# Optimization experiments

Hardware: AMD Instinct MI355X
Metric: run time of the kernel (lower is better)

## Reference

```python
import jax, jax.numpy as jnp
import numpy as np

N_NODES = 20000
DIM = 512
N_EDGES = 320000  # first N_NODES edges are self-loops so every node has a predecessor
EPS = 1e-7


def _logmap0(y):
    # Poincare ball (c=1) log map at origin: artanh(||y||) * y / ||y||
    n = jnp.linalg.norm(y, axis=-1, keepdims=True)
    nc = jnp.clip(n, EPS, 1.0 - 1e-6)
    return jnp.arctanh(nc) * y / nc


def _expmap0(v):
    # Poincare ball (c=1) exp map at origin: tanh(||v||) * v / ||v||
    n = jnp.linalg.norm(v, axis=-1, keepdims=True)
    nc = jnp.maximum(n, EPS)
    return jnp.tanh(nc) * v / nc


def setup_inputs() -> dict:
    key = jax.random.key(0)
    ks = jax.random.split(key, 9)
    x_raw = jax.random.normal(ks[0], (N_NODES, DIM), dtype=jnp.float32)
    nrm = jnp.linalg.norm(x_raw, axis=-1, keepdims=True)
    x = 0.7 * x_raw / (1.0 + nrm)  # strictly inside the unit ball

    rng = np.random.RandomState(0)
    src_rand = rng.randint(0, N_NODES, size=N_EDGES - N_NODES)
    dst_rand = rng.randint(0, N_NODES, size=N_EDGES - N_NODES)
    loop = np.arange(N_NODES)
    src = jnp.asarray(np.concatenate([loop, src_rand]), dtype=jnp.int32)
    dst = jnp.asarray(np.concatenate([loop, dst_rand]), dtype=jnp.int32)

    s = 1.0 / np.sqrt(DIM)
    Wq = jax.random.normal(ks[1], (DIM, DIM), jnp.float32) * s
    bq = jax.random.normal(ks[2], (DIM,), jnp.float32) * 0.01
    Wk = jax.random.normal(ks[3], (DIM, DIM), jnp.float32) * s
    bk = jax.random.normal(ks[4], (DIM,), jnp.float32) * 0.01
    Wv = jax.random.normal(ks[5], (DIM, DIM), jnp.float32) * s
    bv = jax.random.normal(ks[6], (DIM,), jnp.float32) * 0.01
    Wo = jax.random.normal(ks[7], (DIM, DIM), jnp.float32) * s
    bo = jax.random.normal(ks[8], (DIM,), jnp.float32) * 0.01
    return dict(x=x, src=src, dst=dst, Wq=Wq, bq=bq, Wk=Wk, bk=bk,
                Wv=Wv, bv=bv, Wo=Wo, bo=bo)


def reference(x, src, dst, Wq, bq, Wk, bk, Wv, bv, Wo, bo):
    n_nodes, d = x.shape
    scale = 1.0 / jnp.sqrt(jnp.asarray(d, x.dtype))

    t = _logmap0(x)                                  # [N, d] tangent vectors
    q = (t @ Wq.T + bq) * scale                      # torch MHA scales q
    k = t @ Wk.T + bk
    v = t @ Wv.T + bv

    # Per-destination attention over predecessor (src) neighbors.
    scores = jnp.sum(q[dst] * k[src], axis=-1)       # [E]
    m = jax.ops.segment_max(scores, dst, num_segments=n_nodes)
    e = jnp.exp(scores - m[dst])
    denom = jax.ops.segment_sum(e, dst, num_segments=n_nodes)
    alpha = e / denom[dst]                           # [E] softmax weights

    attn = jax.ops.segment_sum(alpha[:, None] * v[src], dst,
                               num_segments=n_nodes)  # [N, d]
    new_h = attn @ Wo.T + bo                          # MHA output projection
    return _expmap0(new_h)
```

## Files before the change

### kernel.cpp

```cpp
#include <hip/hip_runtime.h>
#include <math.h>
#include <stdint.h>

#define NND 20000
#define DIMK 512
#define NE  320000

typedef __attribute__((ext_vector_type(8))) short short8;
typedef __attribute__((ext_vector_type(4))) float floatx4;

__device__ inline float bf2f(unsigned short h) {
    unsigned int u = ((unsigned int)h) << 16;
    return __uint_as_float(u);
}
__device__ inline unsigned short f2bf(float f) {
    unsigned int u = __float_as_uint(f);
    unsigned int r = (u + 0x7fffu + ((u >> 16) & 1u)) >> 16;
    return (unsigned short)r;
}

__device__ __forceinline__ void gld_lds16(const unsigned short* g, unsigned short* l) {
    __builtin_amdgcn_global_load_lds(
        (const __attribute__((address_space(1))) void*)g,
        (__attribute__((address_space(3))) void*)l,
        16, 0, 0);
}

__global__ __launch_bounds__(256) void k_pre(const float* __restrict__ x,
                                             const float* __restrict__ Wq,
                                             const float* __restrict__ Wk,
                                             const float* __restrict__ Wv,
                                             const float* __restrict__ Wo,
                                             const float* __restrict__ bq,
                                             const float* __restrict__ bv,
                                             const float* __restrict__ bo,
                                             const int* __restrict__ dst,
                                             int* __restrict__ counts,
                                             unsigned short* __restrict__ t,
                                             unsigned short* __restrict__ WqTs,
                                             unsigned short* __restrict__ WkT,
                                             unsigned short* __restrict__ WvT,
                                             unsigned short* __restrict__ WoB,
                                             float* __restrict__ bh,
                                             float* __restrict__ bpr,
                                             float scf) {
    int blk = blockIdx.x, tid = threadIdx.x;
    if (blk < 5000) {
        int row = blk * 4 + (tid >> 6);
        int lane = tid & 63;
        const floatx4* xp = (const floatx4*)(x + (size_t)row * DIMK + lane * 8);
        floatx4 x0 = xp[0], x1 = xp[1];
        float ss = 0.f;
#pragma unroll
        for (int i = 0; i < 4; i++) { ss += x0[i] * x0[i]; ss += x1[i] * x1[i]; }
#pragma unroll
        for (int off = 32; off >= 1; off >>= 1) ss += __shfl_xor(ss, off, 64);
        float n  = sqrtf(ss);
        float nc = fminf(fmaxf(n, 1e-7f), 1.0f - 1e-6f);
        float fac = atanhf(nc) / nc;
        union { short8 v; unsigned short u[8]; } o;
#pragma unroll
        for (int i = 0; i < 4; i++) { o.u[i] = f2bf(fac * x0[i]); o.u[4 + i] = f2bf(fac * x1[i]); }
        *(short8*)(t + (size_t)row * DIMK + lane * 8) = o.v;
    } else if (blk < 5256) {
        int i = (blk - 5000) * 256 + tid;
        floatx4 f = *(const floatx4*)(Wo + (size_t)i * 4);
        union { unsigned long long d; unsigned short u[4]; } o;
#pragma unroll
        for (int q = 0; q < 4; q++) o.u[q] = f2bf(f[q]);
        *(unsigned long long*)(WoB + (size_t)i * 4) = o.d;
    } else if (blk < 5448) {
        int g = blk - 5256;
        int m = g >> 6, tile = g & 63;
        int tr = tile >> 3, tc = tile & 7;
        const float* srcm = (m == 0) ? Wq : (m == 1) ? Wk : Wv;
        unsigned short* dstp = (m == 0) ? WqTs : (m == 1) ? WkT : WvT;
        float sc = (m == 0) ? scf : 1.0f;
        __shared__ float tl[64][65];
#pragma unroll
        for (int i = 0; i < 16; i++) {
            int idx = i * 256 + tid; int r = idx >> 6, c = idx & 63;
            tl[c][r] = srcm[(size_t)(tr * 64 + r) * 512 + tc * 64 + c];
        }
        __syncthreads();
#pragma unroll
        for (int i = 0; i < 16; i++) {
            int idx = i * 256 + tid; int r = idx >> 6, c = idx & 63;
            dstp[(size_t)(tc * 64 + r) * 512 + tr * 64 + c] = f2bf(tl[r][c] * sc);
        }
    } else if (blk < 5450) {
        int col = (blk - 5448) * 256 + tid;
        float s = 0.f;
#pragma unroll 8
        for (int m = 0; m < 512; m++) s += bq[m] * Wk[(size_t)m * 512 + col];
        bh[col] = s * scf;
    } else if (blk < 5578) {
        int row = (blk - 5450) * 4 + (tid >> 6);
        int lane = tid & 63;
        const floatx4* wp = (const floatx4*)(Wo + (size_t)row * 512 + lane * 8);
        const floatx4* bp = (const floatx4*)(bv + lane * 8);
        floatx4 a0 = wp[0], a1 = wp[1], c0 = bp[0], c1 = bp[1];
        float s = 0.f;
#pragma unroll
        for (int i = 0; i < 4; i++) { s += a0[i] * c0[i]; s += a1[i] * c1[i]; }
#pragma unroll
        for (int off = 32; off >= 1; off >>= 1) s += __shfl_xor(s, off, 64);
        if (lane == 0) bpr[row] = s + bo[row];
    } else {
        int e = (blk - 5578) * 256 + tid;
        if (e < NE) atomicAdd(&counts[dst[e]], 1);
    }
}

__global__ __launch_bounds__(256) void k_gemm(const unsigned short* __restrict__ A,
                                              const unsigned short* __restrict__ B,
                                              const float* __restrict__ biasf,
                                              unsigned short* __restrict__ out_q,
                                              float* __restrict__ out_f,
                                              int M, int MT, int NT, int Ncols) {
    __shared__ unsigned short smem[16384];
    int b = blockIdx.x;
    int xcd = b & 7, i = b >> 3;
    int nt = i % NT, mt = (i / NT) * 8 + xcd;
    if (mt >= MT) return;
    int m0 = mt * 128, n0 = nt * 128;
    int tid = threadIdx.x, wv = tid >> 6, ln = tid & 63;
    int lr = ln & 15, qd = ln >> 4;
    int mh = wv >> 1, nh = wv & 1;

    floatx4 acc[4][4] = {};
    int srow = wv * 16 + (ln >> 2);
    int scol = (((ln & 3) ^ (ln >> 4)) & 3) * 8;
    int fsw = (qd ^ (lr >> 2)) & 3;

    {
        unsigned short* Ab = smem;
        unsigned short* Bb = smem + 8192;
#pragma unroll
        for (int p = 0; p < 2; p++) {
            int tr = p * 64 + srow;
            int ar = m0 + tr; if (ar > M - 1) ar = M - 1;
            gld_lds16(A + (size_t)ar * DIMK + scol, Ab + (p * 64 + wv * 16) * 32);
            gld_lds16(B + (size_t)(n0 + tr) * DIMK + scol, Bb + (p * 64 + wv * 16) * 32);
        }
    }

    for (int it = 0; it < 16; it++) {
        int cur = it & 1, nxt = cur ^ 1;
        __syncthreads();
        if (it + 1 < 16) {
            int kb = (it + 1) * 32;
            unsigned short* Ab = smem + nxt * 4096;
            unsigned short* Bb = smem + 8192 + nxt * 4096;
#pragma unroll
            for (int p = 0; p < 2; p++) {
                int tr = p * 64 + srow;
                int ar = m0 + tr; if (ar > M - 1) ar = M - 1;
                gld_lds16(A + (size_t)ar * DIMK + kb + scol, Ab + (p * 64 + wv * 16) * 32);
                gld_lds16(B + (size_t)(n0 + tr) * DIMK + kb + scol, Bb + (p * 64 + wv * 16) * 32);
            }
        }
        const unsigned short* Ac = smem + cur * 4096;
        const unsigned short* Bc = smem + 8192 + cur * 4096;
        short8 af[4], bfr[4];
#pragma unroll
        for (int mi = 0; mi < 4; mi++)
            af[mi] = *(const short8*)(Ac + (mh * 64 + mi * 16 + lr) * 32 + fsw * 8);
#pragma unroll
        for (int ni = 0; ni < 4; ni++)
            bfr[ni] = *(const short8*)(Bc + (nh * 64 + ni * 16 + lr) * 32 + fsw * 8);
#pragma unroll
        for (int mi = 0; mi < 4; mi++)
#pragma unroll
            for (int ni = 0; ni < 4; ni++)
                acc[mi][ni] = __builtin_amdgcn_mfma_f32_16x16x32_bf16(af[mi], bfr[ni], acc[mi][ni], 0, 0, 0);
    }

    float bb[4];
#pragma unroll
    for (int ni = 0; ni < 4; ni++) bb[ni] = biasf[n0 + nh * 64 + ni * 16 + lr];

    if (!out_f) {
        int col0 = nt * 128;
        unsigned short* cs = smem;
#pragma unroll
        for (int g = 0; g < 4; g++) {
            __syncthreads();
            if (mh == (g >> 1)) {
                int miB = (g & 1) * 2;
#pragma unroll
                for (int m2 = 0; m2 < 2; m2++) {
                    int mi = miB + m2;
                    int lrow = mi * 16 + qd * 4 - (g & 1) * 32;
#pragma unroll
                    for (int ni = 0; ni < 4; ni++) {
                        int col = nh * 64 + ni * 16 + lr;
#pragma unroll
                        for (int r = 0; r < 4; r++)
                            cs[(lrow + r) * 128 + col] = f2bf(acc[mi][ni][r] + bb[ni]);
                    }
                }
            }
            __syncthreads();
#pragma unroll
            for (int itr = 0; itr < 2; itr++) {
                int slot = itr * 256 + tid;
                int row = slot >> 4, cg = slot & 15;
                int gm = m0 + g * 32 + row;
                if (gm < M) {
                    short8 vv = *(const short8*)(cs + row * 128 + cg * 8);
                    *(short8*)(out_q + (size_t)gm * 512 + col0 + cg * 8) = vv;
                }
            }
        }
    } else {
#pragma unroll
        for (int ni = 0; ni < 4; ni++) {
            int gn = n0 + nh * 64 + ni * 16 + lr;
#pragma unroll
            for (int mi = 0; mi < 4; mi++) {
                int gm0 = m0 + mh * 64 + mi * 16 + qd * 4;
#pragma unroll
                for (int r = 0; r < 4; r++) {
                    int gm = gm0 + r;
                    if (gm < M) out_f[(size_t)gm * Ncols + gn] = acc[mi][ni][r] + bb[ni];
                }
            }
        }
    }
}

__global__ __launch_bounds__(1024) void k_scan(const int* __restrict__ counts,
                                               int* __restrict__ offsets,
                                               int* __restrict__ pos) {
    const int C = 20;
    __shared__ int wsum[16];
    __shared__ int wpre[16];
    int tid = threadIdx.x, lane = tid & 63, w = tid >> 6;
    int local[C];
    int run = 0;
#pragma unroll
    for (int i = 0; i < C; i++) {
        int idx = tid * C + i;
        int c = (idx < NND) ? counts[idx] : 0;
        local[i] = run; run += c;
    }
    int v = run;
#pragma unroll
    for (int off = 1; off < 64; off <<= 1) {
        int u = __shfl_up(v, off, 64);
        if (lane >= off) v += u;
    }
    if (lane == 63) wsum[w] = v;
    __syncthreads();
    if (tid == 0) { int acc = 0; for (int i = 0; i < 16; i++) { wpre[i] = acc; acc += wsum[i]; } }
    __syncthreads();
    int texcl = wpre[w] + (v - run);
#pragma unroll
    for (int i = 0; i < C; i++) {
        int idx = tid * C + i;
        if (idx < NND) { int o = texcl + local[i]; offsets[idx] = o; pos[idx] = o; }
    }
    if (tid == 1023) offsets[NND] = texcl + run;
}

__global__ __launch_bounds__(256) void k_scatter(const int* __restrict__ dst,
                                                 const int* __restrict__ src,
                                                 int* __restrict__ pos,
                                                 int* __restrict__ ssrc,
                                                 const unsigned short* __restrict__ WkT,
                                                 const unsigned short* __restrict__ WqTs,
                                                 const unsigned short* __restrict__ WoB,
                                                 const unsigned short* __restrict__ WvT,
                                                 unsigned short* __restrict__ Amat,
                                                 unsigned short* __restrict__ Wovb) {
    __shared__ unsigned short smem[16384];
    int b = blockIdx.x;
    if (b < 1250) {
        int e = b * 256 + threadIdx.x;
        if (e < NE) { int p = atomicAdd(&pos[dst[e]], 1); ssrc[p] = src[e]; }
        return;
    }
    int g = b - 1250;
    int prod = g >> 4;
    int mt = (g >> 2) & 3, nt = g & 3;
    const unsigned short* A = prod ? WoB : WkT;
    const unsigned short* B = prod ? WvT : WqTs;
    unsigned short* outp = prod ? Wovb : Amat;
    int m0 = mt * 128, n0 = nt * 128;
    int tid = threadIdx.x, wv = tid >> 6, ln = tid & 63;
    int lr = ln & 15, qd = ln >> 4;
    int mh = wv >> 1, nh = wv & 1;
    floatx4 acc[4][4] = {};
    int srow = wv * 16 + (ln >> 2);
    int scol = (((ln & 3) ^ (ln >> 4)) & 3) * 8;
    int fsw = (qd ^ (lr >> 2)) & 3;
    {
        unsigned short* Ab = smem;
        unsigned short* Bb = smem + 8192;
#pragma unroll
        for (int p = 0; p < 2; p++) {
            int tr = p * 64 + srow;
            gld_lds16(A + (size_t)(m0 + tr) * DIMK + scol, Ab + (p * 64 + wv * 16) * 32);
            gld_lds16(B + (size_t)(n0 + tr) * DIMK + scol, Bb + (p * 64 + wv * 16) * 32);
        }
    }
    for (int it = 0; it < 16; it++) {
        int cur = it & 1, nxt = cur ^ 1;
        __syncthreads();
        if (it + 1 < 16) {
            int kb = (it + 1) * 32;
            unsigned short* Ab = smem + nxt * 4096;
            unsigned short* Bb = smem + 8192 + nxt * 4096;
#pragma unroll
            for (int p = 0; p < 2; p++) {
                int tr = p * 64 + srow;
                gld_lds16(A + (size_t)(m0 + tr) * DIMK + kb + scol, Ab + (p * 64 + wv * 16) * 32);
                gld_lds16(B + (size_t)(n0 + tr) * DIMK + kb + scol, Bb + (p * 64 + wv * 16) * 32);
            }
        }
        const unsigned short* Ac = smem + cur * 4096;
        const unsigned short* Bc = smem + 8192 + cur * 4096;
        short8 af[4], bfr[4];
#pragma unroll
        for (int mi = 0; mi < 4; mi++)
            af[mi] = *(const short8*)(Ac + (mh * 64 + mi * 16 + lr) * 32 + fsw * 8);
#pragma unroll
        for (int ni = 0; ni < 4; ni++)
            bfr[ni] = *(const short8*)(Bc + (nh * 64 + ni * 16 + lr) * 32 + fsw * 8);
#pragma unroll
        for (int mi = 0; mi < 4; mi++)
#pragma unroll
            for (int ni = 0; ni < 4; ni++)
                acc[mi][ni] = __builtin_amdgcn_mfma_f32_16x16x32_bf16(af[mi], bfr[ni], acc[mi][ni], 0, 0, 0);
    }
#pragma unroll
    for (int ni = 0; ni < 4; ni++) {
        int gn = n0 + nh * 64 + ni * 16 + lr;
#pragma unroll
        for (int mi = 0; mi < 4; mi++) {
            int gm0 = m0 + mh * 64 + mi * 16 + qd * 4;
#pragma unroll
            for (int r = 0; r < 4; r++)
                outp[(size_t)(gm0 + r) * 512 + gn] = f2bf(acc[mi][ni][r]);
        }
    }
}

__global__ __launch_bounds__(256) void k_fsa(const int* __restrict__ offsets,
                                             const int* __restrict__ ssrc,
                                             const unsigned short* __restrict__ qb,
                                             const unsigned short* __restrict__ tb,
                                             unsigned short* __restrict__ attn) {
    __shared__ float sacc[4][512];
    __shared__ float sden[4];
    int n = blockIdx.x, tid = threadIdx.x, wv = tid >> 6, ln = tid & 63;
    int beg = offsets[n], end = offsets[n + 1];
    union { short8 v; unsigned short u[8]; } qu;
    qu.v = *(const short8*)(qb + (size_t)n * 512 + ln * 8);
    float qf[8];
#pragma unroll
    for (int j = 0; j < 8; j++) qf[j] = bf2f(qu.u[j]);
    float av[8] = {0, 0, 0, 0, 0, 0, 0, 0};
    float den = 0.f;
    int i = beg + wv * 2;
    for (; i + 1 < end; i += 8) {
        const unsigned short* p0 = tb + (size_t)ssrc[i] * 512 + ln * 8;
        const unsigned short* p1 = tb + (size_t)ssrc[i + 1] * 512 + ln * 8;
        union { short8 v; unsigned short u[8]; } r0, r1;
        r0.v = *(const short8*)p0;
        r1.v = *(const short8*)p1;
        float t0[8], t1[8];
        float d0 = 0.f, d1 = 0.f;
#pragma unroll
        for (int j = 0; j < 8; j++) {
            t0[j] = bf2f(r0.u[j]); d0 += qf[j] * t0[j];
            t1[j] = bf2f(r1.u[j]); d1 += qf[j] * t1[j];
        }
#pragma unroll
        for (int off = 32; off >= 1; off >>= 1) {
            d0 += __shfl_xor(d0, off, 64);
            d1 += __shfl_xor(d1, off, 64);
        }
        float w0 = __expf(d0), w1 = __expf(d1);
        den += w0 + w1;
#pragma unroll
        for (int j = 0; j < 8; j++) av[j] += w0 * t0[j] + w1 * t1[j];
    }
    if (i < end) {
        const unsigned short* p0 = tb + (size_t)ssrc[i] * 512 + ln * 8;
        union { short8 v; unsigned short u[8]; } r0;
        r0.v = *(const short8*)p0;
        float t0[8];
        float d0 = 0.f;
#pragma unroll
        for (int j = 0; j < 8; j++) { t0[j] = bf2f(r0.u[j]); d0 += qf[j] * t0[j]; }
#pragma unroll
        for (int off = 32; off >= 1; off >>= 1) d0 += __shfl_xor(d0, off, 64);
        float w0 = __expf(d0);
        den += w0;
#pragma unroll
        for (int j = 0; j < 8; j++) av[j] += w0 * t0[j];
    }
    floatx4 s0v = {av[0], av[1], av[2], av[3]};
    floatx4 s1v = {av[4], av[5], av[6], av[7]};
    *(floatx4*)&sacc[wv][ln * 8]     = s0v;
    *(floatx4*)&sacc[wv][ln * 8 + 4] = s1v;
    if (ln == 0) sden[wv] = den;
    __syncthreads();
    float inv = 1.0f / (sden[0] + sden[1] + sden[2] + sden[3]);
    int c = tid * 2;
    float t0 = sacc[0][c] + sacc[1][c] + sacc[2][c] + sacc[3][c];
    float t1 = sacc[0][c + 1] + sacc[1][c + 1] + sacc[2][c + 1] + sacc[3][c + 1];
    attn[(size_t)n * 512 + c]     = f2bf(t0 * inv);
    attn[(size_t)n * 512 + c + 1] = f2bf(t1 * inv);
}

__global__ __launch_bounds__(64) void k_expmap(float* h) {
    int row = blockIdx.x, lane = threadIdx.x;
    floatx4* hp = (floatx4*)(h + (size_t)row * DIMK + lane * 8);
    floatx4 h0 = hp[0], h1 = hp[1];
    float ss = 0.f;
#pragma unroll
    for (int i = 0; i < 4; i++) { ss += h0[i] * h0[i]; ss += h1[i] * h1[i]; }
#pragma unroll
    for (int off = 32; off >= 1; off >>= 1) ss += __shfl_xor(ss, off, 64);
    float n  = sqrtf(ss);
    float nc = fmaxf(n, 1e-7f);
    float fac = tanhf(nc) / nc;
#pragma unroll
    for (int i = 0; i < 4; i++) { h0[i] *= fac; h1[i] *= fac; }
    hp[0] = h0; hp[1] = h1;
}

extern "C" void kernel_launch(void* const* d_in, const int* in_sizes, int n_in,
                              void* d_out, int out_size, void* d_ws, size_t ws_size,
                              hipStream_t stream) {
    const float* x  = (const float*)d_in[0];
    const int* src  = (const int*)d_in[1];
    const int* dst  = (const int*)d_in[2];
    const float* Wq = (const float*)d_in[3];
    const float* bq = (const float*)d_in[4];
    const float* Wk = (const float*)d_in[5];
    const float* Wv = (const float*)d_in[7];
    const float* bv = (const float*)d_in[8];
    const float* Wo = (const float*)d_in[9];
    const float* bo = (const float*)d_in[10];
    float* out = (float*)d_out;

    char* ws = (char*)d_ws;
    const size_t RB  = (size_t)NND * DIMK * 2;
    const size_t WB  = (size_t)DIMK * DIMK * 2;
    unsigned short* t    = (unsigned short*)(ws);
    unsigned short* qh   = (unsigned short*)(ws + RB);
    unsigned short* WqTs = (unsigned short*)(ws + 2 * RB);
    unsigned short* WkT  = (unsigned short*)(ws + 2 * RB + WB);
    unsigned short* WvT  = (unsigned short*)(ws + 2 * RB + 2 * WB);
    unsigned short* WoB  = (unsigned short*)(ws + 2 * RB + 3 * WB);
    unsigned short* Amat = (unsigned short*)(ws + 2 * RB + 4 * WB);
    unsigned short* Wovb = (unsigned short*)(ws + 2 * RB + 5 * WB);
    float* bh            = (float*)(ws + 2 * RB + 6 * WB);
    float* bpr           = (float*)(ws + 2 * RB + 6 * WB + 2048);
    char* p = ws + 2 * RB + 6 * WB + 4096;
    int* ssrc    = (int*)p;
    int* counts  = ssrc + NE;
    int* offsets = counts + NND;
    int* pos     = offsets + NND + 2;
    unsigned short* attn = qh;

    hipMemsetAsync(counts, 0, (size_t)NND * 4, stream);

    const float scf = 0.04419417382415922f;
    k_pre<<<6828, 256, 0, stream>>>(x, Wq, Wk, Wv, Wo, bq, bv, bo, dst, counts,
                                    t, WqTs, WkT, WvT, WoB, bh, bpr, scf);

    k_scan<<<1, 1024, 0, stream>>>(counts, offsets, pos);
    k_scatter<<<1282, 256, 0, stream>>>(dst, src, pos, ssrc,
                                        WkT, WqTs, WoB, WvT, Amat, Wovb);

    k_gemm<<<8 * 20 * 4, 256, 0, stream>>>(t, Amat, bh, qh, nullptr,
                                           NND, 157, 4, 512);

    k_fsa<<<NND, 256, 0, stream>>>(offsets, ssrc, qh, t, attn);

    k_gemm<<<8 * 20 * 4, 256, 0, stream>>>(attn, Wovb, bpr, nullptr, out,
                                           NND, 157, 4, 512);
    k_expmap<<<NND, 64, 0, stream>>>(out);
}
```

Baseline: 285.1 us.

## Merge scan with weight products, overlap scatter with Q GEMM, regroup attention lanes

The single-block scan is folded into the weight-product kernel as block 0, using 256 threads over 79 counts each. The CSR scatter is launched in the same grid as the query GEMM so the two independent stages share one launch. The per-node attention kernel now splits each wave into four 16-lane groups, so 16 edges are processed concurrently per block with 32 elements per lane and a 4-step shuffle reduction. It uses packed float2 math and a padded LDS transpose for the final reduction, trading more registers for fewer shuffles and more memory-level parallelism on the gathers.

```diff
diff --git a/kernel.cpp b/kernel.cpp
--- a/kernel.cpp
+++ b/kernel.cpp
@@ -8,6 +8,7 @@
 
 typedef __attribute__((ext_vector_type(8))) short short8;
 typedef __attribute__((ext_vector_type(4))) float floatx4;
+typedef __attribute__((ext_vector_type(2))) float float2v;
 
 __device__ inline float bf2f(unsigned short h) {
     unsigned int u = ((unsigned int)h) << 16;
@@ -17,6 +18,12 @@
     unsigned int u = __float_as_uint(f);
     unsigned int r = (u + 0x7fffu + ((u >> 16) & 1u)) >> 16;
     return (unsigned short)r;
+}
+__device__ __forceinline__ float2v up2(unsigned int u) {
+    float2v r;
+    r.x = __uint_as_float(u << 16);
+    r.y = __uint_as_float(u & 0xFFFF0000u);
+    return r;
 }
 
 __device__ __forceinline__ void gld_lds16(const unsigned short* g, unsigned short* l) {
@@ -112,15 +119,15 @@
     }
 }
 
-__global__ __launch_bounds__(256) void k_gemm(const unsigned short* __restrict__ A,
-                                              const unsigned short* __restrict__ B,
-                                              const float* __restrict__ biasf,
-                                              unsigned short* __restrict__ out_q,
-                                              float* __restrict__ out_f,
-                                              int M, int MT, int NT, int Ncols) {
-    __shared__ unsigned short smem[16384];
-    int b = blockIdx.x;
-    int xcd = b & 7, i = b >> 3;
+__device__ __forceinline__ void gemm_tile(int vb,
+                                          const unsigned short* __restrict__ A,
+                                          const unsigned short* __restrict__ B,
+                                          const float* __restrict__ biasf,
+                                          unsigned short* __restrict__ out_q,
+                                          float* __restrict__ out_f,
+                                          int M, int MT, int NT, int Ncols,
+                                          unsigned short* smem) {
+    int xcd = vb & 7, i = vb >> 3;
     int nt = i % NT, mt = (i / NT) * 8 + xcd;
     if (mt >= MT) return;
     int m0 = mt * 128, n0 = nt * 128;
@@ -230,65 +237,56 @@
     }
 }
 
-__global__ __launch_bounds__(1024) void k_scan(const int* __restrict__ counts,
-                                               int* __restrict__ offsets,
-                                               int* __restrict__ pos) {
-    const int C = 20;
-    __shared__ int wsum[16];
-    __shared__ int wpre[16];
-    int tid = threadIdx.x, lane = tid & 63, w = tid >> 6;
-    int local[C];
-    int run = 0;
-#pragma unroll
-    for (int i = 0; i < C; i++) {
-        int idx = tid * C + i;
-        int c = (idx < NND) ? counts[idx] : 0;
-        local[i] = run; run += c;
-    }
-    int v = run;
-#pragma unroll
-    for (int off = 1; off < 64; off <<= 1) {
-        int u = __shfl_up(v, off, 64);
-        if (lane >= off) v += u;
-    }
-    if (lane == 63) wsum[w] = v;
-    __syncthreads();
-    if (tid == 0) { int acc = 0; for (int i = 0; i < 16; i++) { wpre[i] = acc; acc += wsum[i]; } }
-    __syncthreads();
-    int texcl = wpre[w] + (v - run);
-#pragma unroll
-    for (int i = 0; i < C; i++) {
-        int idx = tid * C + i;
-        if (idx < NND) { int o = texcl + local[i]; offsets[idx] = o; pos[idx] = o; }
-    }
-    if (tid == 1023) offsets[NND] = texcl + run;
-}
-
-__global__ __launch_bounds__(256) void k_scatter(const int* __restrict__ dst,
-                                                 const int* __restrict__ src,
-                                                 int* __restrict__ pos,
-                                                 int* __restrict__ ssrc,
-                                                 const unsigned short* __restrict__ WkT,
-                                                 const unsigned short* __restrict__ WqTs,
-                                                 const unsigned short* __restrict__ WoB,
-                                                 const unsigned short* __restrict__ WvT,
-                                                 unsigned short* __restrict__ Amat,
-                                                 unsigned short* __restrict__ Wovb) {
+__global__ __launch_bounds__(256) void k_scan33(const int* __restrict__ counts,
+                                                int* __restrict__ offsets,
+                                                int* __restrict__ pos,
+                                                const unsigned short* __restrict__ WkT,
+                                                const unsigned short* __restrict__ WqTs,
+                                                const unsigned short* __restrict__ WoB,
+                                                const unsigned short* __restrict__ WvT,
+                                                unsigned short* __restrict__ Amat,
+                                                unsigned short* __restrict__ Wovb) {
     __shared__ unsigned short smem[16384];
-    int b = blockIdx.x;
-    if (b < 1250) {
-        int e = b * 256 + threadIdx.x;
-        if (e < NE) { int p = atomicAdd(&pos[dst[e]], 1); ssrc[p] = src[e]; }
+    int tid = threadIdx.x;
+    if (blockIdx.x == 0) {
+        const int CPT = 79;
+        int base = tid * CPT;
+        int tot = 0;
+        for (int i = 0; i < CPT; i++) {
+            int idx = base + i;
+            tot += (idx < NND) ? counts[idx] : 0;
+        }
+        int lane = tid & 63, w = tid >> 6;
+        int v = tot;
+#pragma unroll
+        for (int off = 1; off < 64; off <<= 1) {
+            int u = __shfl_up(v, off, 64);
+            if (lane >= off) v += u;
+        }
+        int* wsum = (int*)smem;
+        if (lane == 63) wsum[w] = v;
+        __syncthreads();
+        int wbase = 0;
+#pragma unroll
+        for (int i = 0; i < 4; i++) wbase += (i < w) ? wsum[i] : 0;
+        int run = wbase + (v - tot);
+        for (int i = 0; i < CPT; i++) {
+            int idx = base + i;
+            if (idx < NND) {
+                offsets[idx] = run; pos[idx] = run;
+                run += counts[idx];
+            }
+        }
         return;
     }
-    int g = b - 1250;
+    int g = blockIdx.x - 1;
     int prod = g >> 4;
     int mt = (g >> 2) & 3, nt = g & 3;
     const unsigned short* A = prod ? WoB : WkT;
     const unsigned short* B = prod ? WvT : WqTs;
     unsigned short* outp = prod ? Wovb : Amat;
     int m0 = mt * 128, n0 = nt * 128;
-    int tid = threadIdx.x, wv = tid >> 6, ln = tid & 63;
+    int wv = tid >> 6, ln = tid & 63;
     int lr = ln & 15, qd = ln >> 4;
     int mh = wv >> 1, nh = wv & 1;
     floatx4 acc[4][4] = {};
@@ -347,73 +345,113 @@
     }
 }
 
+__global__ __launch_bounds__(256) void k_sg(const unsigned short* __restrict__ t,
+                                            const unsigned short* __restrict__ Amat,
+                                            const float* __restrict__ bh,
+                                            unsigned short* __restrict__ qh,
+                                            const int* __restrict__ dst,
+                                            const int* __restrict__ src,
+                                            int* __restrict__ pos,
+                                            int* __restrict__ ssrc) {
+    __shared__ unsigned short smem[16384];
+    int b = blockIdx.x;
+    if (b < 640) {
+        gemm_tile(b, t, Amat, bh, qh, nullptr, NND, 157, 4, 512, smem);
+    } else {
+        int e = (b - 640) * 256 + threadIdx.x;
+        if (e < NE) { int p = atomicAdd(&pos[dst[e]], 1); ssrc[p] = src[e]; }
+    }
+}
+
+__global__ __launch_bounds__(256) void k_proj(const unsigned short* __restrict__ A,
+                                              const unsigned short* __restrict__ B,
+                                              const float* __restrict__ biasf,
+                                              float* __restrict__ out_f) {
+    __shared__ unsigned short smem[16384];
+    gemm_tile(blockIdx.x, A, B, biasf, nullptr, out_f, NND, 157, 4, 512, smem);
+}
+
 __global__ __launch_bounds__(256) void k_fsa(const int* __restrict__ offsets,
+                                             const int* __restrict__ counts,
                                              const int* __restrict__ ssrc,
                                              const unsigned short* __restrict__ qb,
                                              const unsigned short* __restrict__ tb,
                                              unsigned short* __restrict__ attn) {
-    __shared__ float sacc[4][512];
+    __shared__ float sacc[4][32][17];
     __shared__ float sden[4];
-    int n = blockIdx.x, tid = threadIdx.x, wv = tid >> 6, ln = tid & 63;
-    int beg = offsets[n], end = offsets[n + 1];
-    union { short8 v; unsigned short u[8]; } qu;
-    qu.v = *(const short8*)(qb + (size_t)n * 512 + ln * 8);
-    float qf[8];
-#pragma unroll
-    for (int j = 0; j < 8; j++) qf[j] = bf2f(qu.u[j]);
-    float av[8] = {0, 0, 0, 0, 0, 0, 0, 0};
+    int n = blockIdx.x, tid = threadIdx.x;
+    int wv = tid >> 6, ln = tid & 63;
+    int grp = ln >> 4, li = ln & 15;
+    int slot = wv * 4 + grp;
+    int beg = offsets[n], end = beg + counts[n];
+
+    const uint4* qp = (const uint4*)(qb + (size_t)n * 512 + li * 32);
+    uint4 qa = qp[0], qb4 = qp[1], qc = qp[2], qd4 = qp[3];
+    float2v q2[16];
+    q2[0] = up2(qa.x);  q2[1] = up2(qa.y);  q2[2] = up2(qa.z);  q2[3] = up2(qa.w);
+    q2[4] = up2(qb4.x); q2[5] = up2(qb4.y); q2[6] = up2(qb4.z); q2[7] = up2(qb4.w);
+    q2[8] = up2(qc.x);  q2[9] = up2(qc.y);  q2[10] = up2(qc.z); q2[11] = up2(qc.w);
+    q2[12] = up2(qd4.x); q2[13] = up2(qd4.y); q2[14] = up2(qd4.z); q2[15] = up2(qd4.w);
+
+    float2v av2[16];
+#pragma unroll
+    for (int i = 0; i < 16; i++) av2[i] = (float2v){0.f, 0.f};
     float den = 0.f;
-    int i = beg + wv * 2;
-    for (; i + 1 < end; i += 8) {
-        const unsigned short* p0 = tb + (size_t)ssrc[i] * 512 + ln * 8;
-        const unsigned short* p1 = tb + (size_t)ssrc[i + 1] * 512 + ln * 8;
-        union { short8 v; unsigned short u[8]; } r0, r1;
-        r0.v = *(const short8*)p0;
-        r1.v = *(const short8*)p1;
-        float t0[8], t1[8];
-        float d0 = 0.f, d1 = 0.f;
-#pragma unroll
-        for (int j = 0; j < 8; j++) {
-            t0[j] = bf2f(r0.u[j]); d0 += qf[j] * t0[j];
-            t1[j] = bf2f(r1.u[j]); d1 += qf[j] * t1[j];
-        }
-#pragma unroll
-        for (int off = 32; off >= 1; off >>= 1) {
-            d0 += __shfl_xor(d0, off, 64);
-            d1 += __shfl_xor(d1, off, 64);
-        }
-        float w0 = __expf(d0), w1 = __expf(d1);
-        den += w0 + w1;
-#pragma unroll
-        for (int j = 0; j < 8; j++) av[j] += w0 * t0[j] + w1 * t1[j];
-    }
-    if (i < end) {
-        const unsigned short* p0 = tb + (size_t)ssrc[i] * 512 + ln * 8;
-        union { short8 v; unsigned short u[8]; } r0;
-        r0.v = *(const short8*)p0;
-        float t0[8];
-        float d0 = 0.f;
-#pragma unroll
-        for (int j = 0; j < 8; j++) { t0[j] = bf2f(r0.u[j]); d0 += qf[j] * t0[j]; }
-#pragma unroll
-        for (int off = 32; off >= 1; off >>= 1) d0 += __shfl_xor(d0, off, 64);
-        float w0 = __expf(d0);
-        den += w0;
-#pragma unroll
-        for (int j = 0; j < 8; j++) av[j] += w0 * t0[j];
-    }
-    floatx4 s0v = {av[0], av[1], av[2], av[3]};
-    floatx4 s1v = {av[4], av[5], av[6], av[7]};
-    *(floatx4*)&sacc[wv][ln * 8]     = s0v;
-    *(floatx4*)&sacc[wv][ln * 8 + 4] = s1v;
+
+    for (int e = beg + slot; e < end; e += 16) {
+        int row = ssrc[e];
+        const uint4* tp = (const uint4*)(tb + (size_t)row * 512 + li * 32);
+        uint4 ta = tp[0], tb4 = tp[1], tc = tp[2], td = tp[3];
+        float2v t0 = up2(ta.x),  t1 = up2(ta.y),  t2 = up2(ta.z),  t3 = up2(ta.w);
+        float2v t4 = up2(tb4.x), t5 = up2(tb4.y), t6 = up2(tb4.z), t7 = up2(tb4.w);
+        float2v t8 = up2(tc.x),  t9 = up2(tc.y),  t10 = up2(tc.z), t11 = up2(tc.w);
+        float2v t12 = up2(td.x), t13 = up2(td.y), t14 = up2(td.z), t15 = up2(td.w);
+        float2v d2 = q2[0] * t0;
+        d2 += q2[1] * t1;   d2 += q2[2] * t2;   d2 += q2[3] * t3;
+        d2 += q2[4] * t4;   d2 += q2[5] * t5;   d2 += q2[6] * t6;
+        d2 += q2[7] * t7;   d2 += q2[8] * t8;   d2 += q2[9] * t9;
+        d2 += q2[10] * t10; d2 += q2[11] * t11; d2 += q2[12] * t12;
+        d2 += q2[13] * t13; d2 += q2[14] * t14; d2 += q2[15] * t15;
+        float d = d2.x + d2.y;
+        d += __shfl_xor(d, 1, 64);
+        d += __shfl_xor(d, 2, 64);
+        d += __shfl_xor(d, 4, 64);
+        d += __shfl_xor(d, 8, 64);
+        float w = __expf(d);
+        den += w;
+        float2v w2 = {w, w};
+        av2[0] += w2 * t0;   av2[1] += w2 * t1;   av2[2] += w2 * t2;
+        av2[3] += w2 * t3;   av2[4] += w2 * t4;   av2[5] += w2 * t5;
+        av2[6] += w2 * t6;   av2[7] += w2 * t7;   av2[8] += w2 * t8;
+        av2[9] += w2 * t9;   av2[10] += w2 * t10; av2[11] += w2 * t11;
+        av2[12] += w2 * t12; av2[13] += w2 * t13; av2[14] += w2 * t14;
+        av2[15] += w2 * t15;
+    }
+#pragma unroll
+    for (int off = 16; off < 64; off <<= 1) {
+        den += __shfl_xor(den, off, 64);
+#pragma unroll
+        for (int i = 0; i < 16; i++) {
+            av2[i].x += __shfl_xor(av2[i].x, off, 64);
+            av2[i].y += __shfl_xor(av2[i].y, off, 64);
+        }
+    }
+    if (grp == 0) {
+#pragma unroll
+        for (int i = 0; i < 16; i++) {
+            sacc[wv][2 * i][li]     = av2[i].x;
+            sacc[wv][2 * i + 1][li] = av2[i].y;
+        }
+    }
     if (ln == 0) sden[wv] = den;
     __syncthreads();
     float inv = 1.0f / (sden[0] + sden[1] + sden[2] + sden[3]);
     int c = tid * 2;
-    float t0 = sacc[0][c] + sacc[1][c] + sacc[2][c] + sacc[3][c];
-    float t1 = sacc[0][c + 1] + sacc[1][c + 1] + sacc[2][c + 1] + sacc[3][c + 1];
-    attn[(size_t)n * 512 + c]     = f2bf(t0 * inv);
-    attn[(size_t)n * 512 + c + 1] = f2bf(t1 * inv);
+    int l0 = c >> 5, e0 = c & 31;
+    float o0 = sacc[0][e0][l0] + sacc[1][e0][l0] + sacc[2][e0][l0] + sacc[3][e0][l0];
+    float o1 = sacc[0][e0 + 1][l0] + sacc[1][e0 + 1][l0] + sacc[2][e0 + 1][l0] + sacc[3][e0 + 1][l0];
+    attn[(size_t)n * 512 + c]     = f2bf(o0 * inv);
+    attn[(size_t)n * 512 + c + 1] = f2bf(o1 * inv);
 }
 
 __global__ __launch_bounds__(64) void k_expmap(float* h) {
@@ -474,16 +512,13 @@
     k_pre<<<6828, 256, 0, stream>>>(x, Wq, Wk, Wv, Wo, bq, bv, bo, dst, counts,
                                     t, WqTs, WkT, WvT, WoB, bh, bpr, scf);
 
-    k_scan<<<1, 1024, 0, stream>>>(counts, offsets, pos);
-    k_scatter<<<1282, 256, 0, stream>>>(dst, src, pos, ssrc,
-                                        WkT, WqTs, WoB, WvT, Amat, Wovb);
-
-    k_gemm<<<8 * 20 * 4, 256, 0, stream>>>(t, Amat, bh, qh, nullptr,
-                                           NND, 157, 4, 512);
-
-    k_fsa<<<NND, 256, 0, stream>>>(offsets, ssrc, qh, t, attn);
-
-    k_gemm<<<8 * 20 * 4, 256, 0, stream>>>(attn, Wovb, bpr, nullptr, out,
-                                           NND, 157, 4, 512);
+    k_scan33<<<33, 256, 0, stream>>>(counts, offsets, pos,
+                                     WkT, WqTs, WoB, WvT, Amat, Wovb);
+
+    k_sg<<<640 + 1250, 256, 0, stream>>>(t, Amat, bh, qh, dst, src, pos, ssrc);
+
+    k_fsa<<<NND, 256, 0, stream>>>(offsets, counts, ssrc, qh, t, attn);
+
+    k_proj<<<640, 256, 0, stream>>>(attn, Wovb, bpr, out);
     k_expmap<<<NND, 64, 0, stream>>>(out);
 }
```

Result: slower. 345.9 us (+21.3%).
